# Performance work log

Measured on AMD Instinct MI355X. Metric: run time of the kernel, lower is better.

The kernel has to match this reference:

```python
import jax, jax.numpy as jnp
import numpy as np

N = 100000
E = 1600000
IN_DIM, HID, H_IN, OUT_DIM, H_OUT = 128, 32, 2, 1, 1
NEG_SLOPE = 0.2


def gat_conv(x, W, a_src, a_dst, b, src, dst, concat):
    """PyG-style GATConv. x:[N,F_in], W:[F_in,H*C], a_*:[H,C], b:[H*C] or [C]."""
    H, C = a_src.shape
    h = (x @ W).reshape(N, H, C)
    asrc = jnp.einsum('nhc,hc->nh', h, a_src)   # [N,H]
    adst = jnp.einsum('nhc,hc->nh', h, a_dst)   # [N,H]
    e = jax.nn.leaky_relu(asrc[src] + adst[dst], NEG_SLOPE)  # [E',H]
    # segment softmax over incoming edges of each destination node
    m = jax.ops.segment_max(e, dst, num_segments=N)
    p = jnp.exp(e - m[dst])
    s = jax.ops.segment_sum(p, dst, num_segments=N)
    alpha = p / s[dst]                           # [E',H]
    out = jax.ops.segment_sum(alpha[:, :, None] * h[src], dst, num_segments=N)  # [N,H,C]
    out = out.reshape(N, H * C) if concat else out.mean(axis=1)
    return out + b


def setup_inputs() -> dict:
    key = jax.random.key(0)
    ks = jax.random.split(key, 16)
    def glorot(k, shape):
        fan = sum(shape[-2:]) if len(shape) > 1 else shape[-1]
        return jax.random.normal(k, shape, jnp.float32) * (2.0 / fan) ** 0.5
    node_attrs = jax.random.normal(ks[0], (N, IN_DIM), jnp.float32)
    edge_index = jax.random.randint(ks[1], (2, E), 0, N, jnp.int64 if jax.config.jax_enable_x64 else jnp.int32)
    params = {
        'W_in':  glorot(ks[2], (IN_DIM, H_IN * HID)),
        'a_src_in': glorot(ks[3], (H_IN, HID)),
        'a_dst_in': glorot(ks[4], (H_IN, HID)),
        'b_in':  jnp.zeros((H_IN * HID,), jnp.float32),
        'W_mid': glorot(ks[5], (H_IN * HID, H_IN * HID)),
        'a_src_mid': glorot(ks[6], (H_IN, HID)),
        'a_dst_mid': glorot(ks[7], (H_IN, HID)),
        'b_mid': jnp.zeros((H_IN * HID,), jnp.float32),
        'W_out': glorot(ks[8], (H_IN * HID, H_OUT * OUT_DIM)),
        'a_src_out': glorot(ks[9], (H_OUT, OUT_DIM)),
        'a_dst_out': glorot(ks[10], (H_OUT, OUT_DIM)),
        'b_out': jnp.zeros((OUT_DIM,), jnp.float32),
    }
    return {'node_attrs': node_attrs, 'edge_index': edge_index, **params}


def reference(node_attrs, edge_index,
              W_in, a_src_in, a_dst_in, b_in,
              W_mid, a_src_mid, a_dst_mid, b_mid,
              W_out, a_src_out, a_dst_out, b_out):
    # add self loops (PyG GATConv default add_self_loops=True)
    loops = jnp.arange(N, dtype=edge_index.dtype)
    src = jnp.concatenate([edge_index[0], loops])
    dst = jnp.concatenate([edge_index[1], loops])

    x = gat_conv(node_attrs, W_in, a_src_in, a_dst_in, b_in, src, dst, True)
    initial_x = x
    x = jax.nn.elu(x)
    for _ in range(6):  # conv_mid reused 6 times with SHARED weights, as in source
        x = gat_conv(x, W_mid, a_src_mid, a_dst_mid, b_mid, src, dst, True) + initial_x
        x = jax.nn.elu(x)
    x = gat_conv(x, W_out, a_src_out, a_dst_out, b_out, src, dst, False)
    return jax.nn.sigmoid(x)
```

## Files before the change

### kernel.cpp

```cpp
#include <hip/hip_runtime.h>
#include <hip/hip_fp16.h>
#include <cmath>

#define NN 100000
#define EE 1600000
#define TOTE (EE + NN)
#define SHIFT 10
#define NBUK 98
#define CAPB 18432
#define SLACK 5632
#define SPAN (TOTE + NBUK * SLACK)
#define PCAP2 40
#define GB 1563
#define XB ((SPAN + 255) / 256)

typedef _Float16 half8_t __attribute__((ext_vector_type(8)));
typedef _Float16 half4_t __attribute__((ext_vector_type(4)));
typedef float float4_t __attribute__((ext_vector_type(4)));

__device__ __forceinline__ float lrelu(float v) { return v > 0.f ? v : 0.2f * v; }

__global__ __launch_bounds__(256) void binA(const int* __restrict__ src, const int* __restrict__ dst,
                                            int* __restrict__ gcur, int* __restrict__ region) {
    __shared__ int cnt[NBUK], gbase[NBUK], pos[NBUK];
    int t = threadIdx.x;
    if (t < NBUK) cnt[t] = 0;
    __syncthreads();
    const int CH = (TOTE + gridDim.x - 1) / gridDim.x;
    int lo = blockIdx.x * CH;
    int hi = lo + CH; if (hi > TOTE) hi = TOTE;
    for (int e = lo + t; e < hi; e += 256) {
        int d = (e < EE) ? dst[e] : (e - EE);
        atomicAdd(&cnt[d >> SHIFT], 1);
    }
    __syncthreads();
    if (t < NBUK) {
        gbase[t] = atomicAdd(&gcur[t], cnt[t]);
        pos[t] = 0;
    }
    __syncthreads();
    for (int e = lo + t; e < hi; e += 256) {
        int s, d;
        if (e < EE) { s = src[e]; d = dst[e]; }
        else        { s = e - EE; d = s; }
        int b = d >> SHIFT;
        int k = atomicAdd(&pos[b], 1);
        region[(size_t)b * CAPB + gbase[b] + k] = (s << SHIFT) | (d & 1023);
    }
}

__global__ __launch_bounds__(1024) void binB(const int* __restrict__ region, const int* __restrict__ gcur,
                                             int2* __restrict__ rng, int* __restrict__ esrc,
                                             int* __restrict__ hist) {
    __shared__ int ncur[1024];
    __shared__ int wsum[16];
    __shared__ int sg[NBUK];
    __shared__ int dh[64];
    __shared__ int sBase;
    int b = blockIdx.x, t = threadIdx.x;
    int n0 = b << SHIFT;
    if (t < NBUK) sg[t] = gcur[t];
    if (t < 64) dh[t] = 0;
    ncur[t] = 0;
    __syncthreads();
    if (t == 0) {
        int run = 0;
        for (int bb = 0; bb < b; ++bb) run += sg[bb] + SLACK;
        sBase = run;
    }
    int cntE = gcur[b];
    const int* reg = region + (size_t)b * CAPB;
    __syncthreads();
    for (int i = t; i < cntE; i += 1024)
        atomicAdd(&ncur[reg[i] & 1023], 1);
    int base = sBase;
    __syncthreads();
    int v = ncur[t];
    int vp = (v + 7) & ~7;
    if (n0 + t < NN) atomicAdd(&dh[v > 63 ? 63 : v], 1);
    __syncthreads();
    int incl = vp;
    for (int off = 1; off < 64; off <<= 1) {
        int u = __shfl_up(incl, off);
        if ((t & 63) >= off) incl += u;
    }
    if ((t & 63) == 63) wsum[t >> 6] = incl;
    __syncthreads();
    if (t < 16) {
        int w = wsum[t];
        int winc = w;
        for (int off = 1; off < 16; off <<= 1) {
            int u = __shfl_up(winc, off);
            if (t >= off) winc += u;
        }
        wsum[t] = winc - w;
    }
    __syncthreads();
    int excl = incl - vp + wsum[t >> 6];
    int start = base + excl;
    int n = n0 + t;
    if (n < NN) rng[n] = make_int2(start, v);
    ncur[t] = start;
    __syncthreads();
    for (int i = t; i < cntE; i += 1024) {
        int p = reg[i];
        int local = p & 1023;
        int k = atomicAdd(&ncur[local], 1);
        esrc[k] = p >> SHIFT;
    }
    __syncthreads();
    if (n < NN) {
        for (int k = start + v; k < start + vp; ++k) esrc[k] = 0;
    }
    if (t < 64) atomicAdd(&hist[t], dh[t]);
}

__global__ __launch_bounds__(256) void scanPrep(const int* __restrict__ hist, int* __restrict__ off,
                                                const float* __restrict__ Wg, _Float16* __restrict__ Wp) {
    int t = threadIdx.x;
    if (blockIdx.x == 0) {
        if (t < 64) {
            int v = hist[t];
            int incl = v;
            for (int o = 1; o < 64; o <<= 1) {
                int u = __shfl_up(incl, o);
                if (t >= o) incl += u;
            }
            off[t] = incl - v;
        }
    } else {
        for (int i = t; i < 64 * 72; i += 256) {
            int row = i / 72, col = i - row * 72;
            _Float16 v = (_Float16)0.f;
            if (col < 64) {
                int k = (col & 3) * 16 + (col >> 2);
                v = (_Float16)Wg[k * 64 + row];
            }
            Wp[i] = v;
        }
    }
}

__global__ __launch_bounds__(256) void degSort(const int2* __restrict__ rng, int* __restrict__ off,
                                               int* __restrict__ perm, int* __restrict__ inv,
                                               int2* __restrict__ rng2) {
    __shared__ int cnt[64], base[64], pos[64];
    int t = threadIdx.x;
    if (t < 64) cnt[t] = 0;
    __syncthreads();
    int n = blockIdx.x * 256 + t;
    int d = 63;
    int2 r = make_int2(0, 0);
    if (n < NN) {
        r = rng[n];
        d = r.y > 63 ? 63 : r.y;
        atomicAdd(&cnt[d], 1);
    }
    __syncthreads();
    if (t < 64) { base[t] = atomicAdd(&off[t], cnt[t]); pos[t] = 0; }
    __syncthreads();
    if (n < NN) {
        int k = atomicAdd(&pos[d], 1);
        int slot = base[d] + k;
        perm[slot] = n;
        inv[n] = slot;
        rng2[slot] = r;
    }
}

__global__ __launch_bounds__(256) void gemm128_xlat(const float* __restrict__ X, const float* __restrict__ W,
                                                    const int* __restrict__ perm,
                                                    const float* __restrict__ a_src, const float* __restrict__ a_dst,
                                                    _Float16* __restrict__ H, float* __restrict__ asrc,
                                                    float* __restrict__ adst,
                                                    const int* __restrict__ esrc, const int* __restrict__ inv,
                                                    int* __restrict__ esrc2) {
    __shared__ _Float16 wt[64][136];
    int bid = blockIdx.x;
    int t = threadIdx.x;
    if (bid >= GB) {
        int k = (bid - GB) * 256 + t;
        if (k < SPAN) {
            unsigned v = (unsigned)esrc[k];
            if (v >= NN) v = 0;
            esrc2[k] = inv[v];
        }
        return;
    }
    for (int it = 0; it < 8; ++it) {
        int idx4 = it * 256 + t;
        int k = idx4 >> 4;
        int n4 = (idx4 * 4) & 63;
        float4 v = *(const float4*)(W + (size_t)idx4 * 4);
        wt[n4 + 0][k] = (_Float16)v.x;
        wt[n4 + 1][k] = (_Float16)v.y;
        wt[n4 + 2][k] = (_Float16)v.z;
        wt[n4 + 3][k] = (_Float16)v.w;
    }
    __syncthreads();

    int row0 = bid * 64;
    int wr = (t >> 6) * 16;
    int lane = t & 63;
    int m = lane & 15;
    int q = lane >> 4;

    int rowA = row0 + wr + m;
    if (rowA >= NN) rowA = NN - 1;
    int srow = perm[rowA];

    float4_t acc[4] = { {0,0,0,0}, {0,0,0,0}, {0,0,0,0}, {0,0,0,0} };
#pragma unroll
    for (int kc = 0; kc < 4; ++kc) {
        const float* xrow = X + (size_t)srow * 128 + q * 8;
        float4 u0 = *(const float4*)(xrow + kc * 32);
        float4 u1 = *(const float4*)(xrow + kc * 32 + 4);
        half8_t av;
        av[0] = (_Float16)u0.x; av[1] = (_Float16)u0.y;
        av[2] = (_Float16)u0.z; av[3] = (_Float16)u0.w;
        av[4] = (_Float16)u1.x; av[5] = (_Float16)u1.y;
        av[6] = (_Float16)u1.z; av[7] = (_Float16)u1.w;
#pragma unroll
        for (int c = 0; c < 4; ++c) {
            half8_t bv = *(const half8_t*)&wt[c * 16 + m][kc * 32 + q * 8];
            acc[c] = __builtin_amdgcn_mfma_f32_16x16x32_f16(av, bv, acc[c], 0, 0, 0);
        }
    }

#pragma unroll
    for (int r = 0; r < 4; ++r) {
        int row = row0 + wr + q * 4 + r;
        if (row < NN) {
            half4_t hv = { (_Float16)acc[0][r], (_Float16)acc[1][r],
                           (_Float16)acc[2][r], (_Float16)acc[3][r] };
            *(half4_t*)(H + (size_t)row * 64 + m * 4) = hv;
        }
    }

    float as0 = a_src[m], as1 = a_src[16 + m], as2 = a_src[32 + m], as3 = a_src[48 + m];
    float ad0 = a_dst[m], ad1 = a_dst[16 + m], ad2 = a_dst[32 + m], ad3 = a_dst[48 + m];
#pragma unroll
    for (int r = 0; r < 4; ++r) {
        float s0 = acc[0][r] * as0 + acc[1][r] * as1;
        float s1 = acc[2][r] * as2 + acc[3][r] * as3;
        float d0 = acc[0][r] * ad0 + acc[1][r] * ad1;
        float d1 = acc[2][r] * ad2 + acc[3][r] * ad3;
#pragma unroll
        for (int mk = 1; mk < 16; mk <<= 1) {
            s0 += __shfl_xor(s0, mk);
            s1 += __shfl_xor(s1, mk);
            d0 += __shfl_xor(d0, mk);
            d1 += __shfl_xor(d1, mk);
        }
        int row = row0 + wr + q * 4 + r;
        if (m == 0 && row < NN) {
            asrc[2 * row + 0] = s0;
            asrc[2 * row + 1] = s1;
            adst[2 * row + 0] = d0;
            adst[2 * row + 1] = d1;
        }
    }
}

struct Acc8 { float a[8]; float l0, l1; };

__device__ __forceinline__ void acc4(Acc8& A, float4 p0, float4 p1, float4 p2, float4 p3,
                                     half8_t h0, half8_t h1, half8_t h2, half8_t h3) {
    A.l0 += p0.x + p1.x + p2.x + p3.x;
    A.l1 += p0.y + p1.y + p2.y + p3.y;
#pragma unroll
    for (int q = 0; q < 8; ++q) {
        float w0 = (q & 2) ? p0.y : p0.x;
        float w1 = (q & 2) ? p1.y : p1.x;
        float w2 = (q & 2) ? p2.y : p2.x;
        float w3 = (q & 2) ? p3.y : p3.x;
        A.a[q] += w0 * (float)h0[q] + w1 * (float)h1[q]
                + w2 * (float)h2[q] + w3 * (float)h3[q];
    }
}

template <int MODE>
__global__ __launch_bounds__(256, 6) void edge_agg(const int2* __restrict__ rng2,
                                                const int* __restrict__ esrc2, const _Float16* __restrict__ h,
                                                const float* __restrict__ asrc, const float* __restrict__ adst,
                                                const float* __restrict__ bias, _Float16* __restrict__ ixbuf,
                                                const _Float16* __restrict__ Wp, const float* __restrict__ asg,
                                                const float* __restrict__ adg, _Float16* __restrict__ hN,
                                                float* __restrict__ asrcN, float* __restrict__ adstN,
                                                const float* __restrict__ Wo, const float* __restrict__ a_s,
                                                const float* __restrict__ a_d, float2* __restrict__ ho2,
                                                float* __restrict__ adst_o) {
    __shared__ float4 pLDS[4][8][PCAP2 + 1];
    int bid = gridDim.x - 1 - blockIdx.x;
    int tid = threadIdx.x;
    int wq = tid >> 6;
    int lane = tid & 63;
    int g = lane >> 3;
    int c8 = lane & 7;

    int slot = (bid * 4 + wq) * 8 + g;
    int2 r = rng2[slot];
    int start = r.x, deg = r.y;
    int vp = (deg + 3) & ~3;
    if (vp > PCAP2) vp = PCAP2;
    float2 ad = *(const float2*)(adst + 2 * (size_t)slot);

    for (int j = c8; j < vp; j += 8) {
        float p0 = 0.f, p1 = 0.f;
        int s = 0;
        if (j < deg) {
            s = esrc2[start + j];
            float2 as = *(const float2*)(asrc + 2 * (size_t)s);
            p0 = __expf(fminf(lrelu(as.x + ad.x), 60.f));
            p1 = __expf(fminf(lrelu(as.y + ad.y), 60.f));
        }
        pLDS[wq][g][j] = make_float4(p0, p1, __int_as_float(s), 0.f);
    }

    float bi[8];
#pragma unroll
    for (int q = 0; q < 8; ++q) bi[q] = bias[(q & 3) * 16 + 2 * c8 + (q >> 2)];
    half8_t iv = {};
    if constexpr (MODE != 0) iv = *(const half8_t*)(ixbuf + (size_t)slot * 64 + 8 * c8);
    float wo[8];
    float as0o = 0.f, ad0o = 0.f;
    if constexpr (MODE == 2) {
#pragma unroll
        for (int q = 0; q < 8; ++q) wo[q] = Wo[(q & 3) * 16 + 2 * c8 + (q >> 2)];
        as0o = a_s[0]; ad0o = a_d[0];
    }

    const float4* pb = &pLDS[wq][g][0];
    const _Float16* hb = h + 8 * c8;
    Acc8 A = {};
    float4 pc0 = pb[0], pc1 = pb[1], pc2 = pb[2], pc3 = pb[3];
    half8_t hc0 = *(const half8_t*)(hb + ((size_t)__float_as_int(pc0.z) << 6));
    half8_t hc1 = *(const half8_t*)(hb + ((size_t)__float_as_int(pc1.z) << 6));
    half8_t hc2 = *(const half8_t*)(hb + ((size_t)__float_as_int(pc2.z) << 6));
    half8_t hc3 = *(const half8_t*)(hb + ((size_t)__float_as_int(pc3.z) << 6));
    for (int j = 4; j < vp; j += 4) {
        float4 pn0 = pb[j], pn1 = pb[j + 1], pn2 = pb[j + 2], pn3 = pb[j + 3];
        acc4(A, pc0, pc1, pc2, pc3, hc0, hc1, hc2, hc3);
        half8_t hn0 = *(const half8_t*)(hb + ((size_t)__float_as_int(pn0.z) << 6));
        half8_t hn1 = *(const half8_t*)(hb + ((size_t)__float_as_int(pn1.z) << 6));
        half8_t hn2 = *(const half8_t*)(hb + ((size_t)__float_as_int(pn2.z) << 6));
        half8_t hn3 = *(const half8_t*)(hb + ((size_t)__float_as_int(pn3.z) << 6));
        pc0 = pn0; pc1 = pn1; pc2 = pn2; pc3 = pn3;
        hc0 = hn0; hc1 = hn1; hc2 = hn2; hc3 = hn3;
    }
    acc4(A, pc0, pc1, pc2, pc3, hc0, hc1, hc2, hc3);

    float inv0 = 1.f / A.l0, inv1 = 1.f / A.l1;
    float t[8];
#pragma unroll
    for (int q = 0; q < 8; ++q) t[q] = A.a[q] * ((q & 2) ? inv1 : inv0) + bi[q];
    if constexpr (MODE == 0) {
        half8_t o;
#pragma unroll
        for (int q = 0; q < 8; ++q) o[q] = (_Float16)t[q];
        *(half8_t*)(ixbuf + (size_t)slot * 64 + 8 * c8) = o;
    } else {
#pragma unroll
        for (int q = 0; q < 8; ++q) t[q] += (float)iv[q];
    }
#pragma unroll
    for (int q = 0; q < 8; ++q) t[q] = t[q] > 0.f ? t[q] : __expf(t[q]) - 1.f;

    if constexpr (MODE != 2) {
        _Float16* xs = (_Float16*)&pLDS[wq][0][0];
        half8_t xv;
#pragma unroll
        for (int q = 0; q < 8; ++q) xv[q] = (_Float16)t[q];
        *(half8_t*)(xs + g * 72 + 8 * c8) = xv;
        int m = lane & 15, qq = lane >> 4;
        half8_t bf0[4], bf1[4];
#pragma unroll
        for (int c = 0; c < 4; ++c) {
            const _Float16* wrow = Wp + (c * 16 + m) * 72 + qq * 8;
            bf0[c] = *(const half8_t*)(wrow);
            bf1[c] = *(const half8_t*)(wrow + 32);
        }
        const _Float16* xrow = xs + (m & 7) * 72 + qq * 8;
        half8_t a0 = *(const half8_t*)(xrow);
        half8_t a1 = *(const half8_t*)(xrow + 32);
        float4_t ag[4] = { {0,0,0,0}, {0,0,0,0}, {0,0,0,0}, {0,0,0,0} };
#pragma unroll
        for (int c = 0; c < 4; ++c) {
            ag[c] = __builtin_amdgcn_mfma_f32_16x16x32_f16(a0, bf0[c], ag[c], 0, 0, 0);
            ag[c] = __builtin_amdgcn_mfma_f32_16x16x32_f16(a1, bf1[c], ag[c], 0, 0, 0);
        }
        int base = (bid * 4 + wq) * 8;
#pragma unroll
        for (int rr = 0; rr < 4; ++rr) {
            if (qq < 2) {
                int nr = base + qq * 4 + rr;
                half4_t hv = { (_Float16)ag[0][rr], (_Float16)ag[1][rr],
                               (_Float16)ag[2][rr], (_Float16)ag[3][rr] };
                *(half4_t*)(hN + (size_t)nr * 64 + m * 4) = hv;
            }
        }
        float gs0 = asg[m], gs1 = asg[16 + m], gs2 = asg[32 + m], gs3 = asg[48 + m];
        float gd0 = adg[m], gd1 = adg[16 + m], gd2 = adg[32 + m], gd3 = adg[48 + m];
#pragma unroll
        for (int rr = 0; rr < 4; ++rr) {
            float s0 = ag[0][rr] * gs0 + ag[1][rr] * gs1;
            float s1 = ag[2][rr] * gs2 + ag[3][rr] * gs3;
            float d0 = ag[0][rr] * gd0 + ag[1][rr] * gd1;
            float d1 = ag[2][rr] * gd2 + ag[3][rr] * gd3;
#pragma unroll
            for (int mk = 1; mk < 16; mk <<= 1) {
                s0 += __shfl_xor(s0, mk);
                s1 += __shfl_xor(s1, mk);
                d0 += __shfl_xor(d0, mk);
                d1 += __shfl_xor(d1, mk);
            }
            if (m == 0 && qq < 2) {
                int nr = base + qq * 4 + rr;
                asrcN[2 * nr + 0] = s0;
                asrcN[2 * nr + 1] = s1;
                adstN[2 * nr + 0] = d0;
                adstN[2 * nr + 1] = d1;
            }
        }
    } else {
        float v = 0.f;
#pragma unroll
        for (int q = 0; q < 8; ++q) v += t[q] * wo[q];
        v += __shfl_xor(v, 1);
        v += __shfl_xor(v, 2);
        v += __shfl_xor(v, 4);
        if (c8 == 0) {
            ho2[slot] = make_float2(v, v * as0o);
            adst_o[slot] = v * ad0o;
        }
    }
}

__global__ __launch_bounds__(256) void edge_agg_out(const int* __restrict__ perm, const int2* __restrict__ rng2,
                                                    const int* __restrict__ esrc2, const float2* __restrict__ ho2,
                                                    const float* __restrict__ adst_o, const float* __restrict__ b_out,
                                                    float* __restrict__ out) {
    int bid = gridDim.x - 1 - blockIdx.x;
    int wq = threadIdx.x >> 6;
    int lane = threadIdx.x & 63;
    int g = lane >> 3;
    int c8 = lane & 7;
    int slot = (bid * 4 + wq) * 8 + g;
    int2 r = rng2[slot];
    float adv = adst_o[slot];
    float l = 0.f, acc = 0.f;
    for (int j = c8; j < r.y; j += 8) {
        int s = esrc2[r.x + j];
        float2 v = ho2[s];
        float p = __expf(fminf(lrelu(v.y + adv), 60.f));
        l += p;
        acc = fmaf(p, v.x, acc);
    }
    l += __shfl_xor(l, 1); acc += __shfl_xor(acc, 1);
    l += __shfl_xor(l, 2); acc += __shfl_xor(acc, 2);
    l += __shfl_xor(l, 4); acc += __shfl_xor(acc, 4);
    if (c8 == 0) out[perm[slot]] = 1.f / (1.f + __expf(-(acc / l + b_out[0])));
}

extern "C" void kernel_launch(void* const* d_in, const int* in_sizes, int n_in,
                              void* d_out, int out_size, void* d_ws, size_t ws_size,
                              hipStream_t stream) {
    const float* node_attrs = (const float*)d_in[0];
    const int*   edge_index = (const int*)d_in[1];
    const float* W_in      = (const float*)d_in[2];
    const float* a_src_in  = (const float*)d_in[3];
    const float* a_dst_in  = (const float*)d_in[4];
    const float* b_in      = (const float*)d_in[5];
    const float* W_mid     = (const float*)d_in[6];
    const float* a_src_mid = (const float*)d_in[7];
    const float* a_dst_mid = (const float*)d_in[8];
    const float* b_mid     = (const float*)d_in[9];
    const float* W_out     = (const float*)d_in[10];
    const float* a_src_out = (const float*)d_in[11];
    const float* a_dst_out = (const float*)d_in[12];
    const float* b_out     = (const float*)d_in[13];
    float* out = (float*)d_out;

    const int* srcArr = edge_index;
    const int* dstArr = edge_index + EE;

    char* w = (char*)d_ws;
    auto alloc = [&](size_t bytes) { void* p = (void*)w; w += (bytes + 255) & ~(size_t)255; return p; };
    int2*  rng        = (int2*)alloc((size_t)NN * 8);
    int2*  rng2       = (int2*)alloc((size_t)NN * 8);
    int*   gcur       = (int*)alloc((size_t)NBUK * 4);
    int*   region     = (int*)alloc((size_t)NBUK * CAPB * 4);
    int*   esrc       = (int*)alloc((size_t)SPAN * 4);
    int*   esrc2      = (int*)alloc((size_t)SPAN * 4);
    _Float16* hA      = (_Float16*)alloc((size_t)NN * 64 * 2);
    _Float16* hB      = (_Float16*)alloc((size_t)NN * 64 * 2);
    _Float16* ixbuf   = (_Float16*)alloc((size_t)NN * 64 * 2);
    float* asA        = (float*)alloc((size_t)NN * 2 * 4);
    float* adA        = (float*)alloc((size_t)NN * 2 * 4);
    float* asB        = (float*)alloc((size_t)NN * 2 * 4);
    float* adB        = (float*)alloc((size_t)NN * 2 * 4);
    float2* ho2       = (float2*)alloc((size_t)NN * 8);
    float* adst_o     = (float*)alloc((size_t)NN * 4);
    int*   perm       = (int*)alloc((size_t)NN * 4);
    int*   invp       = (int*)alloc((size_t)NN * 4);
    int*   hist       = (int*)alloc(64 * 4);
    int*   off        = (int*)alloc(64 * 4);
    _Float16* wperm   = (_Float16*)alloc((size_t)64 * 72 * 2);

    hipMemsetAsync(gcur, 0, NBUK * 4, stream);
    hipMemsetAsync(hist, 0, 64 * 4, stream);
    binA<<<256, 256, 0, stream>>>(srcArr, dstArr, gcur, region);
    binB<<<NBUK, 1024, 0, stream>>>(region, gcur, rng, esrc, hist);

    scanPrep<<<2, 256, 0, stream>>>(hist, off, W_mid, wperm);
    int nBlk = (NN + 255) / 256;
    degSort<<<nBlk, 256, 0, stream>>>(rng, off, perm, invp, rng2);

    int aggBlocks = NN / 32;

    gemm128_xlat<<<GB + XB, 256, 0, stream>>>(node_attrs, W_in, perm, a_src_in, a_dst_in,
                                              hA, asA, adA, esrc, invp, esrc2);

    edge_agg<0><<<aggBlocks, 256, 0, stream>>>(rng2, esrc2, hA, asA, adA, b_in, ixbuf,
                                               wperm, a_src_mid, a_dst_mid, hB, asB, adB,
                                               nullptr, nullptr, nullptr, nullptr, nullptr);

    for (int l = 0; l < 5; ++l) {
        _Float16* hs = (l & 1) ? hA : hB;  float* ass = (l & 1) ? asA : asB;  float* ads = (l & 1) ? adA : adB;
        _Float16* hd = (l & 1) ? hB : hA;  float* asd = (l & 1) ? asB : asA;  float* add = (l & 1) ? adB : adA;
        edge_agg<1><<<aggBlocks, 256, 0, stream>>>(rng2, esrc2, hs, ass, ads, b_mid, ixbuf,
                                                   wperm, a_src_mid, a_dst_mid, hd, asd, add,
                                                   nullptr, nullptr, nullptr, nullptr, nullptr);
    }
    edge_agg<2><<<aggBlocks, 256, 0, stream>>>(rng2, esrc2, hA, asA, adA, b_mid, ixbuf,
                                               nullptr, nullptr, nullptr, nullptr, nullptr, nullptr,
                                               W_out, a_src_out, a_dst_out, ho2, adst_o);

    edge_agg_out<<<aggBlocks, 256, 0, stream>>>(perm, rng2, esrc2, ho2, adst_o, b_out, out);
}
```

Before: 496.1 us.

## Use smaller 256-node buckets in CSR build and fold scan into degree sort

The binning preprocessing now splits destinations into 391 buckets of 256 nodes instead of 98 buckets of 1024 nodes. The second binning pass can then run 391 blocks of 256 threads rather than 98 blocks of 1024, which spreads the work over more compute units. The separate scanPrep kernel is removed: every degSort block recomputes the 64-entry histogram scan, and one extra block does the weight permutation. The two memsets are merged into a single one. This saves a launch and improves occupancy in the CSR build, in exchange for redundant scans and tighter per-bucket capacity margins.

Result: no change. 495.6 us (-0.1%).

```diff
diff --git a/kernel.cpp b/kernel.cpp
--- a/kernel.cpp
+++ b/kernel.cpp
@@ -5,10 +5,11 @@
 #define NN 100000
 #define EE 1600000
 #define TOTE (EE + NN)
-#define SHIFT 10
-#define NBUK 98
-#define CAPB 18432
-#define SLACK 5632
+#define SHIFT 8
+#define BSZ 256
+#define NBUK 391
+#define CAPB 5120
+#define SLACK 1792
 #define SPAN (TOTE + NBUK * SLACK)
 #define PCAP2 40
 #define GB 1563
@@ -24,7 +25,7 @@
                                             int* __restrict__ gcur, int* __restrict__ region) {
     __shared__ int cnt[NBUK], gbase[NBUK], pos[NBUK];
     int t = threadIdx.x;
-    if (t < NBUK) cnt[t] = 0;
+    for (int i = t; i < NBUK; i += 256) cnt[i] = 0;
     __syncthreads();
     const int CH = (TOTE + gridDim.x - 1) / gridDim.x;
     int lo = blockIdx.x * CH;
@@ -34,9 +35,9 @@
         atomicAdd(&cnt[d >> SHIFT], 1);
     }
     __syncthreads();
-    if (t < NBUK) {
-        gbase[t] = atomicAdd(&gcur[t], cnt[t]);
-        pos[t] = 0;
+    for (int i = t; i < NBUK; i += 256) {
+        gbase[i] = atomicAdd(&gcur[i], cnt[i]);
+        pos[i] = 0;
     }
     __syncthreads();
     for (int e = lo + t; e < hi; e += 256) {
@@ -45,21 +46,21 @@
         else        { s = e - EE; d = s; }
         int b = d >> SHIFT;
         int k = atomicAdd(&pos[b], 1);
-        region[(size_t)b * CAPB + gbase[b] + k] = (s << SHIFT) | (d & 1023);
-    }
-}
-
-__global__ __launch_bounds__(1024) void binB(const int* __restrict__ region, const int* __restrict__ gcur,
-                                             int2* __restrict__ rng, int* __restrict__ esrc,
-                                             int* __restrict__ hist) {
-    __shared__ int ncur[1024];
-    __shared__ int wsum[16];
+        region[(size_t)b * CAPB + gbase[b] + k] = (s << SHIFT) | (d & (BSZ - 1));
+    }
+}
+
+__global__ __launch_bounds__(256) void binB(const int* __restrict__ region, const int* __restrict__ gcur,
+                                            int2* __restrict__ rng, int* __restrict__ esrc,
+                                            int* __restrict__ hist) {
+    __shared__ int ncur[BSZ];
+    __shared__ int wsum[4];
     __shared__ int sg[NBUK];
     __shared__ int dh[64];
     __shared__ int sBase;
     int b = blockIdx.x, t = threadIdx.x;
     int n0 = b << SHIFT;
-    if (t < NBUK) sg[t] = gcur[t];
+    for (int i = t; i < NBUK; i += 256) sg[i] = gcur[i];
     if (t < 64) dh[t] = 0;
     ncur[t] = 0;
     __syncthreads();
@@ -71,8 +72,8 @@
     int cntE = gcur[b];
     const int* reg = region + (size_t)b * CAPB;
     __syncthreads();
-    for (int i = t; i < cntE; i += 1024)
-        atomicAdd(&ncur[reg[i] & 1023], 1);
+    for (int i = t; i < cntE; i += 256)
+        atomicAdd(&ncur[reg[i] & (BSZ - 1)], 1);
     int base = sBase;
     __syncthreads();
     int v = ncur[t];
@@ -86,10 +87,10 @@
     }
     if ((t & 63) == 63) wsum[t >> 6] = incl;
     __syncthreads();
-    if (t < 16) {
+    if (t < 4) {
         int w = wsum[t];
         int winc = w;
-        for (int off = 1; off < 16; off <<= 1) {
+        for (int off = 1; off < 4; off <<= 1) {
             int u = __shfl_up(winc, off);
             if (t >= off) winc += u;
         }
@@ -102,9 +103,9 @@
     if (n < NN) rng[n] = make_int2(start, v);
     ncur[t] = start;
     __syncthreads();
-    for (int i = t; i < cntE; i += 1024) {
+    for (int i = t; i < cntE; i += 256) {
         int p = reg[i];
-        int local = p & 1023;
+        int local = p & (BSZ - 1);
         int k = atomicAdd(&ncur[local], 1);
         esrc[k] = p >> SHIFT;
     }
@@ -115,20 +116,12 @@
     if (t < 64) atomicAdd(&hist[t], dh[t]);
 }
 
-__global__ __launch_bounds__(256) void scanPrep(const int* __restrict__ hist, int* __restrict__ off,
-                                                const float* __restrict__ Wg, _Float16* __restrict__ Wp) {
+__global__ __launch_bounds__(256) void degSort(const int2* __restrict__ rng, const int* __restrict__ hist,
+                                               int* __restrict__ offg, int* __restrict__ perm,
+                                               int* __restrict__ inv, int2* __restrict__ rng2,
+                                               const float* __restrict__ Wg, _Float16* __restrict__ Wp) {
     int t = threadIdx.x;
-    if (blockIdx.x == 0) {
-        if (t < 64) {
-            int v = hist[t];
-            int incl = v;
-            for (int o = 1; o < 64; o <<= 1) {
-                int u = __shfl_up(incl, o);
-                if (t >= o) incl += u;
-            }
-            off[t] = incl - v;
-        }
-    } else {
+    if (blockIdx.x == gridDim.x - 1) {
         for (int i = t; i < 64 * 72; i += 256) {
             int row = i / 72, col = i - row * 72;
             _Float16 v = (_Float16)0.f;
@@ -138,14 +131,9 @@
             }
             Wp[i] = v;
         }
-    }
-}
-
-__global__ __launch_bounds__(256) void degSort(const int2* __restrict__ rng, int* __restrict__ off,
-                                               int* __restrict__ perm, int* __restrict__ inv,
-                                               int2* __restrict__ rng2) {
-    __shared__ int cnt[64], base[64], pos[64];
-    int t = threadIdx.x;
+        return;
+    }
+    __shared__ int cnt[64], base[64], pos[64], excl[64];
     if (t < 64) cnt[t] = 0;
     __syncthreads();
     int n = blockIdx.x * 256 + t;
@@ -156,8 +144,17 @@
         d = r.y > 63 ? 63 : r.y;
         atomicAdd(&cnt[d], 1);
     }
-    __syncthreads();
-    if (t < 64) { base[t] = atomicAdd(&off[t], cnt[t]); pos[t] = 0; }
+    if (t < 64) {
+        int v = hist[t];
+        int incl = v;
+        for (int o = 1; o < 64; o <<= 1) {
+            int u = __shfl_up(incl, o);
+            if (t >= o) incl += u;
+        }
+        excl[t] = incl - v;
+    }
+    __syncthreads();
+    if (t < 64) { base[t] = excl[t] + atomicAdd(&offg[t], cnt[t]); pos[t] = 0; }
     __syncthreads();
     if (n < NN) {
         int k = atomicAdd(&pos[d], 1);
@@ -488,7 +485,7 @@
     auto alloc = [&](size_t bytes) { void* p = (void*)w; w += (bytes + 255) & ~(size_t)255; return p; };
     int2*  rng        = (int2*)alloc((size_t)NN * 8);
     int2*  rng2       = (int2*)alloc((size_t)NN * 8);
-    int*   gcur       = (int*)alloc((size_t)NBUK * 4);
+    int*   zbuf       = (int*)alloc((size_t)(NBUK + 128) * 4);
     int*   region     = (int*)alloc((size_t)NBUK * CAPB * 4);
     int*   esrc       = (int*)alloc((size_t)SPAN * 4);
     int*   esrc2      = (int*)alloc((size_t)SPAN * 4);
@@ -503,18 +500,18 @@
     float* adst_o     = (float*)alloc((size_t)NN * 4);
     int*   perm       = (int*)alloc((size_t)NN * 4);
     int*   invp       = (int*)alloc((size_t)NN * 4);
-    int*   hist       = (int*)alloc(64 * 4);
-    int*   off        = (int*)alloc(64 * 4);
     _Float16* wperm   = (_Float16*)alloc((size_t)64 * 72 * 2);
 
-    hipMemsetAsync(gcur, 0, NBUK * 4, stream);
-    hipMemsetAsync(hist, 0, 64 * 4, stream);
+    int* gcur = zbuf;
+    int* hist = zbuf + NBUK;
+    int* offg = zbuf + NBUK + 64;
+
+    hipMemsetAsync(zbuf, 0, (NBUK + 128) * 4, stream);
     binA<<<256, 256, 0, stream>>>(srcArr, dstArr, gcur, region);
-    binB<<<NBUK, 1024, 0, stream>>>(region, gcur, rng, esrc, hist);
-
-    scanPrep<<<2, 256, 0, stream>>>(hist, off, W_mid, wperm);
+    binB<<<NBUK, 256, 0, stream>>>(region, gcur, rng, esrc, hist);
+
     int nBlk = (NN + 255) / 256;
-    degSort<<<nBlk, 256, 0, stream>>>(rng, off, perm, invp, rng2);
+    degSort<<<nBlk + 1, 256, 0, stream>>>(rng, hist, offg, perm, invp, rng2, W_mid, wperm);
 
     int aggBlocks = NN / 32;
 
```
